# Kernel tuning notes

Measured on AMD Instinct MI355X. Metric: run time of the kernel, lower is better.

## Reference

```python
import jax, jax.numpy as jnp
import numpy as np
from jax import lax

# Constants from the torch module
THRESH = 0.5
SIGMA = 1.0
BIAS = -0.2
C_GAUSS = 0.3989422804014327  # 1/sqrt(2*pi)

@jax.custom_vjp
def lif_act(mem):
    # forward: hard threshold spike
    return (mem > THRESH).astype(mem.dtype)

def _lif_fwd(mem):
    return lif_act(mem), mem

def _lif_bwd(mem, g):
    # Gaussian surrogate gradient (use_gause_approx branch)
    grad = g * (C_GAUSS / SIGMA) * jnp.exp(-0.5 / (SIGMA ** 2) * (mem - THRESH + BIAS) ** 2)
    return (grad,)

lif_act.defvjp(_lif_fwd, _lif_bwd)


def setup_inputs() -> dict:
    key = jax.random.key(0)
    k1, _ = jax.random.split(key)
    # x: [B, C, T, H, W] with time on axis 2
    x = jax.random.normal(k1, (16, 64, 16, 64, 64), dtype=jnp.float32)
    decay = jnp.ones((1,), dtype=jnp.float32) * 0.5
    return {"x": x, "decay": decay}


def reference(x, decay):
    # sigmoid-normalized decay (norm_decay)
    decay_s = jax.nn.sigmoid(decay)  # shape (1,), broadcasts
    xt = jnp.moveaxis(x, 2, 0)       # [T, B, C, H, W]
    zeros = jnp.zeros_like(xt[0])

    def step(carry, x_t):
        mem_old, spike = carry
        # mem = mem_old * sigmoid(decay) * (1 - spike.detach()) + x_t
        # with mem_old=0, spike=0 at t=0 this reduces to mem = x_0, matching torch.
        mem = mem_old * decay_s * (1.0 - lax.stop_gradient(spike)) + x_t
        new_spike = lif_act(mem)
        return (mem, new_spike), new_spike

    _, out = lax.scan(step, (zeros, zeros), xt)  # out: [T, B, C, H, W]
    out = jnp.moveaxis(out, 0, 2)                # [B, C, T, H, W]
    # if_clamp_the_output = True
    return jnp.clip(out, 0.0, 1.0)
```

## Files before the change

### kernel.cpp

```cpp
#include <hip/hip_runtime.h>


#define T_STEPS 16
#define HW      4096
#define BC      1024
#define S4      1024

typedef float f4 __attribute__((ext_vector_type(4)));

__global__ __launch_bounds__(256) void
lif_fwd_kernel(const float* __restrict__ x,
               const float* __restrict__ decay,
               float* __restrict__ out) {
    const unsigned tid = blockIdx.x * blockDim.x + threadIdx.x;
    const unsigned bc  = tid >> 10;
    const unsigned s4  = tid & (S4 - 1);
    const unsigned base = bc * (T_STEPS * HW) + s4 * 4;

    const float d  = decay[0];
    const float ds = 1.0f / (1.0f + expf(-d));

    f4 xv[T_STEPS];
#pragma unroll
    for (int t = 0; t < T_STEPS; ++t) {
        xv[t] = __builtin_nontemporal_load(
            reinterpret_cast<const f4*>(x + base + (unsigned)t * HW));
    }

    float mx = 0.f, my = 0.f, mz = 0.f, mw = 0.f;
    float sx = 0.f, sy = 0.f, sz = 0.f, sw = 0.f;
#pragma unroll
    for (int t = 0; t < T_STEPS; ++t) {
        mx = __fadd_rn(__fmul_rn(__fmul_rn(mx, ds), 1.0f - sx), xv[t].x);
        my = __fadd_rn(__fmul_rn(__fmul_rn(my, ds), 1.0f - sy), xv[t].y);
        mz = __fadd_rn(__fmul_rn(__fmul_rn(mz, ds), 1.0f - sz), xv[t].z);
        mw = __fadd_rn(__fmul_rn(__fmul_rn(mw, ds), 1.0f - sw), xv[t].w);

        sx = (mx > 0.5f) ? 1.0f : 0.0f;
        sy = (my > 0.5f) ? 1.0f : 0.0f;
        sz = (mz > 0.5f) ? 1.0f : 0.0f;
        sw = (mw > 0.5f) ? 1.0f : 0.0f;

        f4 ov;
        ov.x = sx; ov.y = sy; ov.z = sz; ov.w = sw;
        __builtin_nontemporal_store(ov,
            reinterpret_cast<f4*>(out + base + (unsigned)t * HW));
    }
}

extern "C" void kernel_launch(void* const* d_in, const int* in_sizes, int n_in,
                              void* d_out, int out_size, void* d_ws, size_t ws_size,
                              hipStream_t stream) {
    const float* x     = (const float*)d_in[0];
    const float* decay = (const float*)d_in[1];
    float*       out   = (float*)d_out;

    const int block = 256;
    const int grid  = (BC * S4) / block;
    lif_fwd_kernel<<<grid, block, 0, stream>>>(x, decay, out);
}
```

Baseline: 428.0 us.

## Process two columns per thread with an 8-deep rolling load pipeline

Halves the grid so each thread handles two columns in sequence. Each column now keeps only 8 time steps of input in flight in a ring buffer, refilled as the recurrence advances, instead of holding all 16 loads in registers. Launch bounds request 8 blocks per CU. The aim is to cut register use and raise occupancy while still hiding memory latency. The cost is less memory-level parallelism per thread and serial work across the two columns.

```diff
diff --git a/kernel.cpp b/kernel.cpp
--- a/kernel.cpp
+++ b/kernel.cpp
@@ -4,47 +4,61 @@
 #define T_STEPS 16
 #define HW      4096
 #define BC      1024
-#define S4      1024
+#define NCOL    (BC * (HW / 4))
+#define NTHREAD (NCOL / 2)
+#define PIPE    8
 
 typedef float f4 __attribute__((ext_vector_type(4)));
 
-__global__ __launch_bounds__(256) void
+__global__ __launch_bounds__(256, 8) void
 lif_fwd_kernel(const float* __restrict__ x,
                const float* __restrict__ decay,
                float* __restrict__ out) {
     const unsigned tid = blockIdx.x * blockDim.x + threadIdx.x;
-    const unsigned bc  = tid >> 10;
-    const unsigned s4  = tid & (S4 - 1);
-    const unsigned base = bc * (T_STEPS * HW) + s4 * 4;
 
     const float d  = decay[0];
     const float ds = 1.0f / (1.0f + expf(-d));
 
-    f4 xv[T_STEPS];
 #pragma unroll
-    for (int t = 0; t < T_STEPS; ++t) {
-        xv[t] = __builtin_nontemporal_load(
-            reinterpret_cast<const f4*>(x + base + (unsigned)t * HW));
-    }
+    for (int col_pass = 0; col_pass < 2; ++col_pass) {
+        const unsigned col  = tid + (unsigned)col_pass * NTHREAD;
+        const unsigned bc   = col >> 10;
+        const unsigned s4   = col & ((HW / 4) - 1);
+        const unsigned base = bc * (T_STEPS * HW) + s4 * 4;
 
-    float mx = 0.f, my = 0.f, mz = 0.f, mw = 0.f;
-    float sx = 0.f, sy = 0.f, sz = 0.f, sw = 0.f;
+        f4 xv[PIPE];
 #pragma unroll
-    for (int t = 0; t < T_STEPS; ++t) {
-        mx = __fadd_rn(__fmul_rn(__fmul_rn(mx, ds), 1.0f - sx), xv[t].x);
-        my = __fadd_rn(__fmul_rn(__fmul_rn(my, ds), 1.0f - sy), xv[t].y);
-        mz = __fadd_rn(__fmul_rn(__fmul_rn(mz, ds), 1.0f - sz), xv[t].z);
-        mw = __fadd_rn(__fmul_rn(__fmul_rn(mw, ds), 1.0f - sw), xv[t].w);
+        for (int t = 0; t < PIPE; ++t) {
+            xv[t] = __builtin_nontemporal_load(
+                reinterpret_cast<const f4*>(x + base + (unsigned)t * HW));
+        }
 
-        sx = (mx > 0.5f) ? 1.0f : 0.0f;
-        sy = (my > 0.5f) ? 1.0f : 0.0f;
-        sz = (mz > 0.5f) ? 1.0f : 0.0f;
-        sw = (mw > 0.5f) ? 1.0f : 0.0f;
+        float mx = 0.f, my = 0.f, mz = 0.f, mw = 0.f;
+        float sx = 0.f, sy = 0.f, sz = 0.f, sw = 0.f;
 
-        f4 ov;
-        ov.x = sx; ov.y = sy; ov.z = sz; ov.w = sw;
-        __builtin_nontemporal_store(ov,
-            reinterpret_cast<f4*>(out + base + (unsigned)t * HW));
+#pragma unroll
+        for (int t = 0; t < T_STEPS; ++t) {
+            const f4 v = xv[t & (PIPE - 1)];
+            if (t + PIPE < T_STEPS) {
+                xv[t & (PIPE - 1)] = __builtin_nontemporal_load(
+                    reinterpret_cast<const f4*>(x + base + (unsigned)(t + PIPE) * HW));
+            }
+
+            mx = __fadd_rn(__fmul_rn(__fmul_rn(mx, ds), 1.0f - sx), v.x);
+            my = __fadd_rn(__fmul_rn(__fmul_rn(my, ds), 1.0f - sy), v.y);
+            mz = __fadd_rn(__fmul_rn(__fmul_rn(mz, ds), 1.0f - sz), v.z);
+            mw = __fadd_rn(__fmul_rn(__fmul_rn(mw, ds), 1.0f - sw), v.w);
+
+            sx = (mx > 0.5f) ? 1.0f : 0.0f;
+            sy = (my > 0.5f) ? 1.0f : 0.0f;
+            sz = (mz > 0.5f) ? 1.0f : 0.0f;
+            sw = (mw > 0.5f) ? 1.0f : 0.0f;
+
+            f4 ov;
+            ov.x = sx; ov.y = sy; ov.z = sz; ov.w = sw;
+            __builtin_nontemporal_store(ov,
+                reinterpret_cast<f4*>(out + base + (unsigned)t * HW));
+        }
     }
 }
 
@@ -56,6 +70,6 @@
     float*       out   = (float*)d_out;
 
     const int block = 256;
-    const int grid  = (BC * S4) / block;
+    const int grid  = NTHREAD / block;
     lif_fwd_kernel<<<grid, block, 0, stream>>>(x, decay, out);
 }
```

After: 432.2 us. About the same (+1.0%).
